# Performance work log

Hardware: AMD Instinct MI355X
Metric: run time of the kernel (lower is better)

The kernel has to match this reference:

```python
import jax, jax.numpy as jnp
import numpy as np

N = 100000          # nodes
E = 600000          # edges (avg degree ~6, mesh graph)
C_IN = 6            # input features (xyz + normals)
H = 64              # hidden channels per PointTransformerConv
OUT = 10            # out_channels
NEG_SLOPE = 0.01    # F.leaky_relu default slope
IN_DIMS = [C_IN, C_IN + H, C_IN + 2 * H, C_IN + 3 * H]


def _lin(key, fin, fout):
    return jax.random.normal(key, (fin, fout), jnp.float32) / np.float32(np.sqrt(fin))


def setup_inputs() -> dict:
    key = jax.random.key(0)
    ks = jax.random.split(key, 40)
    inp = {
        "x": jax.random.normal(ks[0], (N, C_IN), jnp.float32),
        "edge_index": jax.random.randint(ks[1], (2, E), 0, N, jnp.int32),
    }
    k = 2
    for l, fin in enumerate(IN_DIMS, start=1):
        inp[f"w{l}_lin"] = _lin(ks[k], fin, H); k += 1   # value projection (bias=False)
        inp[f"w{l}_src"] = _lin(ks[k], fin, H); k += 1   # attention src projection
        inp[f"w{l}_dst"] = _lin(ks[k], fin, H); k += 1   # attention dst projection
        inp[f"w{l}_pos"] = _lin(ks[k], fin, H); k += 1   # positional MLP (Linear)
        inp[f"b{l}_pos"] = jnp.zeros((H,), jnp.float32)
    inp["w_mlp1"] = _lin(ks[k], C_IN + 4 * H, H); k += 1
    inp["b_mlp1"] = jnp.zeros((H,), jnp.float32)
    inp["w_mlp2"] = _lin(ks[k], H, OUT); k += 1
    inp["b_mlp2"] = jnp.zeros((OUT,), jnp.float32)
    return inp


def _ptconv(x, src, dst, w_lin, w_src, w_dst, w_pos, b_pos):
    """PointTransformerConv with x serving as both features and positions.
    message = softmax_i(a_dst[i] - a_src[j] + delta_ij) * (h[j] + delta_ij),
    delta_ij = pos_nn(x_i - x_j); sum-aggregated over incoming edges."""
    h = x @ w_lin                                   # [N,H] values
    a_src = x @ w_src                               # [N,H]
    a_dst = x @ w_dst                               # [N,H]
    delta = (x[dst] - x[src]) @ w_pos + b_pos       # [E,H] pos_nn(pos_i - pos_j)
    alpha = a_dst[dst] - a_src[src] + delta         # [E,H] per-edge, per-channel logits
    # numerically stable segment softmax over edges grouped by destination node
    amax = jax.ops.segment_max(alpha, dst, num_segments=N)      # [N,H]
    e = jnp.exp(alpha - amax[dst])                              # [E,H]
    denom = jax.ops.segment_sum(e, dst, num_segments=N)         # [N,H]
    w = e / (denom[dst] + 1e-16)                                # [E,H]
    return jax.ops.segment_sum(w * (h[src] + delta), dst, num_segments=N)  # [N,H]


def _forward(x, edge_index, ps):
    src, dst = edge_index[0], edge_index[1]
    lrelu = lambda v: jnp.where(v > 0, v, NEG_SLOPE * v)
    x1 = _ptconv(x, src, dst, *ps[0])
    x2 = lrelu(_ptconv(jnp.concatenate([x, x1], 1), src, dst, *ps[1]))
    x3 = lrelu(_ptconv(jnp.concatenate([x, x1, x2], 1), src, dst, *ps[2]))
    x4 = lrelu(_ptconv(jnp.concatenate([x, x1, x2, x3], 1), src, dst, *ps[3]))
    out = jnp.concatenate([x, x1, x2, x3, x4], 1)   # [N, 262]
    w_mlp1, b_mlp1, w_mlp2, b_mlp2 = ps[4]
    out = out @ w_mlp1 + b_mlp1                     # dropout = identity (eval mode)
    return out @ w_mlp2 + b_mlp2                    # [N, OUT]


def reference(x, edge_index,
              w1_lin, w1_src, w1_dst, w1_pos, b1_pos,
              w2_lin, w2_src, w2_dst, w2_pos, b2_pos,
              w3_lin, w3_src, w3_dst, w3_pos, b3_pos,
              w4_lin, w4_src, w4_dst, w4_pos, b4_pos,
              w_mlp1, b_mlp1, w_mlp2, b_mlp2):
    ps = [(w1_lin, w1_src, w1_dst, w1_pos, b1_pos),
          (w2_lin, w2_src, w2_dst, w2_pos, b2_pos),
          (w3_lin, w3_src, w3_dst, w3_pos, b3_pos),
          (w4_lin, w4_src, w4_dst, w4_pos, b4_pos),
          (w_mlp1, b_mlp1, w_mlp2, b_mlp2)]
    return _forward(x, edge_index, ps)
```

## Files before the change

### kernel.cpp

```cpp
#include <hip/hip_runtime.h>
#include <hip/hip_fp16.h>

#define NN 100000
#define EE 600000
#define XSB 288
#define SCAN_B 2048
#define LOG2E 1.44269504f

typedef __attribute__((ext_vector_type(8))) short s16x8;
typedef __attribute__((ext_vector_type(4))) float f32x4;

__device__ inline unsigned short f2b(float f) {
    unsigned u = __float_as_uint(f);
    u += 0x7fffu + ((u >> 16) & 1u);
    return (unsigned short)(u >> 16);
}

__device__ inline void wconv_elem(int idx, int fin,
                                  const float* wlin, const float* wsrc,
                                  const float* wpos, unsigned short* wt) {
    int ks = idx / 6144;
    int rem = idx - ks * 6144;
    int col = rem >> 5, kk = rem & 31;
    int k = ks * 32 + kk;
    float val = 0.f;
    if (k < fin) {
        int m = col >> 6, c = col & 63;
        const float* W = (m == 0) ? wlin : (m == 1) ? wsrc : wpos;
        val = W[k * 64 + c];
    }
    wt[idx] = f2b(val);
}

#define O0 600000
#define O1 606144
#define O2 624576
#define O3 655296
#define O4 698304
#define O5 716736
#define O6 1316736
#define O7 1316800

__global__ __launch_bounds__(256) void k_setup(
    const float* __restrict__ x, const int* __restrict__ ei,
    const float* __restrict__ wl0, const float* __restrict__ ws0, const float* __restrict__ wp0,
    const float* __restrict__ wl1, const float* __restrict__ ws1, const float* __restrict__ wp1,
    const float* __restrict__ wl2, const float* __restrict__ ws2, const float* __restrict__ wp2,
    const float* __restrict__ wl3, const float* __restrict__ ws3, const float* __restrict__ wp3,
    const float* __restrict__ w1,
    unsigned short* __restrict__ xb,
    unsigned short* __restrict__ wt0, unsigned short* __restrict__ wt1,
    unsigned short* __restrict__ wt2, unsigned short* __restrict__ wt3,
    unsigned short* __restrict__ w1t, int* __restrict__ deg,
    unsigned* __restrict__ vgu) {
    int i = blockIdx.x * 256 + threadIdx.x;
    if (i < O0) {
        int n = i / 6, c = i - n * 6;
        xb[(size_t)n * XSB + c] = f2b(x[i]);
    } else if (i < O1) {
        wconv_elem(i - O0, 6, wl0, ws0, wp0, wt0);
    } else if (i < O2) {
        wconv_elem(i - O1, 70, wl1, ws1, wp1, wt1);
    } else if (i < O3) {
        wconv_elem(i - O2, 134, wl2, ws2, wp2, wt2);
    } else if (i < O4) {
        wconv_elem(i - O3, 198, wl3, ws3, wp3, wt3);
    } else if (i < O5) {
        int idx = i - O4;
        int col = idx / 288, k = idx - col * 288;
        w1t[idx] = f2b((k < 262) ? w1[k * 64 + col] : 0.f);
    } else if (i < O6) {
        atomicAdd(&deg[ei[EE + (i - O5)]], 1);
    } else if (i < O7) {
        vgu[(size_t)NN * 64 + (i - O6)] = 0u;
    }
}


__global__ void k_scan1(const int* __restrict__ deg, int* __restrict__ rowptr,
                        int* __restrict__ bsum) {
    __shared__ int sh[256];
    int b = blockIdx.x, t = threadIdx.x;
    int base = b * SCAN_B + t * 8;
    int vals[8];
    int s = 0;
#pragma unroll
    for (int j = 0; j < 8; j++) {
        int i = base + j;
        int d = (i < NN) ? deg[i] : 0;
        s += d;
        vals[j] = s;
    }
    sh[t] = s;
    __syncthreads();
    for (int off = 1; off < 256; off <<= 1) {
        int vv = (t >= off) ? sh[t - off] : 0;
        __syncthreads();
        sh[t] += vv;
        __syncthreads();
    }
    int excl = (t > 0) ? sh[t - 1] : 0;
#pragma unroll
    for (int j = 0; j < 8; j++) {
        int i = base + j;
        if (i < NN) rowptr[i + 1] = vals[j] + excl;
    }
    if (t == 255) bsum[b] = sh[255];
}

__global__ void k_scan3m(const int* __restrict__ deg, int* __restrict__ rowptr,
                         const int* __restrict__ bsum, int* __restrict__ cursor) {
    __shared__ int soff;
    int b = blockIdx.x, t = threadIdx.x;
    if (t < 64) {
        int v = (t < b) ? bsum[t] : 0;
#pragma unroll
        for (int m = 1; m < 64; m <<= 1) v += __shfl_xor(v, m);
        if (t == 0) soff = v;
    }
    __syncthreads();
    int off = soff;
    int base = b * SCAN_B + t * 8;
#pragma unroll
    for (int j = 0; j < 8; j++) {
        int i = base + j;
        if (i < NN) {
            int incl = rowptr[i + 1] + off;
            rowptr[i + 1] = incl;
            cursor[i] = incl - deg[i];
        }
    }
    if (b == 0 && t == 0) rowptr[0] = 0;
}

__global__ void k_scatter(const int* __restrict__ ei, int* __restrict__ cursor,
                          int* __restrict__ csrc) {
    int e = blockIdx.x * 256 + threadIdx.x;
    if (e < EE) {
        int d = ei[EE + e];
        int pos = atomicAdd(&cursor[d], 1);
        csrc[pos] = ei[e];
    }
}


template <int KP>
__global__ __launch_bounds__(256) void k_projm(
    const unsigned short* __restrict__ xb, const unsigned short* __restrict__ wt,
    const float* __restrict__ bpos,
    unsigned* __restrict__ vg, __half* __restrict__ qh) {
    __shared__ short wl[192 * 32];
    const int t = threadIdx.x;
    const int w = t >> 6, l = t & 63;
    const int lo = l & 15, hi = l >> 4;
    const int row_w = blockIdx.x * 128 + w * 32;

    f32x4 acc[2][12];
#pragma unroll
    for (int a = 0; a < 2; a++)
#pragma unroll
        for (int i = 0; i < 12; i++) acc[a][i] = (f32x4)0.f;

    const unsigned short* arow0 = xb + (size_t)(row_w + lo) * XSB;
    const unsigned short* arow1 = xb + (size_t)(row_w + 16 + lo) * XSB;
#pragma unroll
    for (int ks = 0; ks < KP / 32; ks++) {
        __syncthreads();
        {
            const uint4* src = (const uint4*)wt + (size_t)ks * 768;
            uint4* dst = (uint4*)wl;
#pragma unroll
            for (int i = 0; i < 3; i++) dst[i * 256 + t] = src[i * 256 + t];
        }
        __syncthreads();
        s16x8 af0 = *(const s16x8*)(arow0 + ks * 32 + hi * 8);
        s16x8 af1 = *(const s16x8*)(arow1 + ks * 32 + hi * 8);
#pragma unroll
        for (int ct = 0; ct < 12; ct++) {
            s16x8 bf = *(const s16x8*)&wl[(ct * 16 + lo) * 32 + hi * 8];
            acc[0][ct] = __builtin_amdgcn_mfma_f32_16x16x32_bf16(af0, bf, acc[0][ct], 0, 0, 0);
            acc[1][ct] = __builtin_amdgcn_mfma_f32_16x16x32_bf16(af1, bf, acc[1][ct], 0, 0, 0);
        }
    }

#pragma unroll
    for (int tile = 0; tile < 2; tile++) {
#pragma unroll
        for (int r = 0; r < 4; r++) {
            int node = row_w + tile * 16 + hi * 4 + r;
            if (node < NN) {
#pragma unroll
                for (int j = 0; j < 4; j++) {
                    int c = j * 16 + lo;
                    float h  = acc[tile][0 + j][r];
                    float as = acc[tile][4 + j][r];
                    float p  = acc[tile][8 + j][r];
                    size_t o = (size_t)node * 64 + c;
                    float P = __builtin_amdgcn_exp2f(-(as + p) * LOG2E);
                    vg[o] = (unsigned)f2b(P) | ((unsigned)f2b(P * (h - p)) << 16);
                    qh[o] = __float2half(p + bpos[c]);
                }
            }
        }
    }
}


__global__ __launch_bounds__(256) void k_mlp1f(
    const unsigned short* __restrict__ xb, const unsigned short* __restrict__ w1t,
    const float* __restrict__ b1, const float* __restrict__ w2,
    const float* __restrict__ b2, float* __restrict__ out) {
    __shared__ float w2l[64][10];
    __shared__ float b2l[10];
    __shared__ float b1l[64];
    for (int t = threadIdx.x; t < 714; t += 256) {
        if (t < 640) ((float*)w2l)[t] = w2[t];
        else if (t < 650) b2l[t - 640] = b2[t - 640];
        else b1l[t - 650] = b1[t - 650];
    }
    __syncthreads();

    const int w = threadIdx.x >> 6, l = threadIdx.x & 63;
    const int lo = l & 15, hi = l >> 4;
    const int row_w = blockIdx.x * 256 + w * 64;

    f32x4 acc[4][4];
#pragma unroll
    for (int a = 0; a < 4; a++)
#pragma unroll
        for (int b = 0; b < 4; b++) acc[a][b] = (f32x4)0.f;

#pragma unroll
    for (int ks = 0; ks < 9; ks++) {
        const int k0 = ks * 32 + hi * 8;
        s16x8 bf[4];
#pragma unroll
        for (int ct = 0; ct < 4; ct++)
            bf[ct] = *(const s16x8*)(w1t + (size_t)(ct * 16 + lo) * 288 + k0);
#pragma unroll
        for (int rt = 0; rt < 4; rt++) {
            s16x8 af = *(const s16x8*)(xb + (size_t)(row_w + rt * 16 + lo) * XSB + k0);
#pragma unroll
            for (int ct = 0; ct < 4; ct++)
                acc[rt][ct] = __builtin_amdgcn_mfma_f32_16x16x32_bf16(af, bf[ct], acc[rt][ct], 0, 0, 0);
        }
    }

#pragma unroll
    for (int rt = 0; rt < 4; rt++) {
#pragma unroll
        for (int r = 0; r < 4; r++) {
            int node = row_w + rt * 16 + hi * 4 + r;
            float po[10];
#pragma unroll
            for (int o = 0; o < 10; o++) po[o] = 0.f;
#pragma unroll
            for (int ct = 0; ct < 4; ct++) {
                int c = ct * 16 + lo;
                float hv = acc[rt][ct][r] + b1l[c];
#pragma unroll
                for (int o = 0; o < 10; o++) po[o] = fmaf(hv, w2l[c][o], po[o]);
            }
#pragma unroll
            for (int m = 1; m < 16; m <<= 1)
#pragma unroll
                for (int o = 0; o < 10; o++) po[o] += __shfl_xor(po[o], m);
            if (lo == 0 && node < NN) {
                float* op = out + (size_t)node * 10;
#pragma unroll
                for (int o = 0; o < 5; o++)
                    *(float2*)(op + o * 2) = make_float2(po[o * 2] + b2l[o * 2],
                                                         po[o * 2 + 1] + b2l[o * 2 + 1]);
            }
        }
    }
}


template <int RELU>
__global__ __launch_bounds__(256) void k_edge(
    const uint4* __restrict__ vg,
    const uint2* __restrict__ qh,
    const int* __restrict__ rowptr, const int* __restrict__ csrc,
    unsigned short* __restrict__ xb, int col) {
    int l = threadIdx.x & 63;
    int g = l >> 4, lg = l & 15;
    int node = (blockIdx.x * 4 + (threadIdx.x >> 6)) * 4 + g;
    int b = rowptr[node], e = rowptr[node + 1];
    int deg = e - b;
    int md = max(deg, __shfl_xor(deg, 16));
    md = max(md, __shfl_xor(md, 32));
    uint2 qr = qh[(size_t)node * 16 + lg];
    float d[4] = {0.f, 0.f, 0.f, 0.f};
    float s[4] = {0.f, 0.f, 0.f, 0.f};
    for (int it = 0; it < md; it += 2) {
        int i0 = NN, i1 = NN;
        if (it < deg)     i0 = csrc[b + it];
        if (it + 1 < deg) i1 = csrc[b + it + 1];
        uint4 r0 = vg[(size_t)i0 * 16 + lg];
        uint4 r1 = vg[(size_t)i1 * 16 + lg];
        const unsigned* u0 = (const unsigned*)&r0;
        const unsigned* u1 = (const unsigned*)&r1;
#pragma unroll
        for (int ch = 0; ch < 4; ch++) {
            d[ch] += __uint_as_float(u0[ch] << 16);
            s[ch] += __uint_as_float(u0[ch] & 0xFFFF0000u);
        }
#pragma unroll
        for (int ch = 0; ch < 4; ch++) {
            d[ch] += __uint_as_float(u1[ch] << 16);
            s[ch] += __uint_as_float(u1[ch] & 0xFFFF0000u);
        }
    }
    float2 q01 = __half22float2(*(const __half2*)&qr.x);
    float2 q23 = __half22float2(*(const __half2*)&qr.y);
    float qv[4] = {q01.x, q01.y, q23.x, q23.y};
    float o[4];
#pragma unroll
    for (int ch = 0; ch < 4; ch++) {
        float v = (s[ch] + qv[ch] * d[ch]) / (d[ch] + 1e-16f);
        if (RELU) v = (v > 0.f) ? v : 0.01f * v;
        o[ch] = v;
    }
    unsigned short* dst = xb + (size_t)node * XSB + col + 4 * lg;
    *(unsigned*)(dst)     = (unsigned)f2b(o[0]) | ((unsigned)f2b(o[1]) << 16);
    *(unsigned*)(dst + 2) = (unsigned)f2b(o[2]) | ((unsigned)f2b(o[3]) << 16);
}


extern "C" void kernel_launch(void* const* d_in, const int* in_sizes, int n_in,
                              void* d_out, int out_size, void* d_ws, size_t ws_size,
                              hipStream_t stream) {
    const float* x = (const float*)d_in[0];
    const int* ei = (const int*)d_in[1];
    const float* W[4][4];
    const float* BP[4];
    int base = 2;
    for (int l = 0; l < 4; l++) {
        for (int m = 0; m < 4; m++) W[l][m] = (const float*)d_in[base + m];
        BP[l] = (const float*)d_in[base + 4];
        base += 5;
    }
    const float* w1 = (const float*)d_in[22];
    const float* b1 = (const float*)d_in[23];
    const float* w2 = (const float*)d_in[24];
    const float* b2 = (const float*)d_in[25];

    char* wsp = (char*)d_ws;
    size_t off = 0;
    auto alloc = [&](size_t bytes) {
        void* p = wsp + off;
        off += (bytes + 255) & ~(size_t)255;
        return p;
    };
    unsigned short* xb = (unsigned short*)alloc((size_t)(NN + 256) * XSB * 2);
    unsigned* vg = (unsigned*)alloc((size_t)(NN + 1) * 64 * 4);
    __half* qh = (__half*)alloc((size_t)NN * 64 * 2);
    int* deg = (int*)alloc((size_t)NN * 4);
    int* rowptr = (int*)alloc((size_t)(NN + 1) * 4);
    int* cursor = (int*)alloc((size_t)NN * 4);
    int* bsum = (int*)alloc(1024 * 4);
    int* csrc = (int*)alloc((size_t)EE * 4);
    const int KPv[4] = {32, 96, 160, 224};
    unsigned short* wt[4];
    for (int l = 0; l < 4; l++) wt[l] = (unsigned short*)alloc((size_t)192 * KPv[l] * 2);
    unsigned short* w1t = (unsigned short*)alloc((size_t)64 * 288 * 2);

    hipMemsetAsync(deg, 0, (size_t)NN * 4, stream);
    k_setup<<<(O7 + 255) / 256, 256, 0, stream>>>(
        x, ei, W[0][0], W[0][1], W[0][3], W[1][0], W[1][1], W[1][3],
        W[2][0], W[2][1], W[2][3], W[3][0], W[3][1], W[3][3], w1,
        xb, wt[0], wt[1], wt[2], wt[3], w1t, deg, vg);

    int nb = (NN + SCAN_B - 1) / SCAN_B;
    k_scan1<<<nb, 256, 0, stream>>>(deg, rowptr, bsum);
    k_scan3m<<<nb, 256, 0, stream>>>(deg, rowptr, bsum, cursor);
    k_scatter<<<(EE + 255) / 256, 256, 0, stream>>>(ei, cursor, csrc);

    const int gProj = (NN + 127) / 128;
    const int gEdge = NN / 16;
    const uint4* vgu = (const uint4*)vg;
    const uint2* qh2 = (const uint2*)qh;

    k_projm<32><<<gProj, 256, 0, stream>>>(xb, wt[0], BP[0], vg, qh);
    k_edge<0><<<gEdge, 256, 0, stream>>>(vgu, qh2, rowptr, csrc, xb, 6);
    k_projm<96><<<gProj, 256, 0, stream>>>(xb, wt[1], BP[1], vg, qh);
    k_edge<1><<<gEdge, 256, 0, stream>>>(vgu, qh2, rowptr, csrc, xb, 70);
    k_projm<160><<<gProj, 256, 0, stream>>>(xb, wt[2], BP[2], vg, qh);
    k_edge<1><<<gEdge, 256, 0, stream>>>(vgu, qh2, rowptr, csrc, xb, 134);
    k_projm<224><<<gProj, 256, 0, stream>>>(xb, wt[3], BP[3], vg, qh);
    k_edge<1><<<gEdge, 256, 0, stream>>>(vgu, qh2, rowptr, csrc, xb, 198);

    k_mlp1f<<<(NN + 255) / 256, 256, 0, stream>>>(xb, w1t, b1, w2, b2, (float*)d_out);
}
```

Baseline: 314.8 us.

## Fuse edge aggregation with next layer projection using ping-pong buffers

```diff
diff --git a/kernel.cpp b/kernel.cpp
--- a/kernel.cpp
+++ b/kernel.cpp
@@ -14,6 +14,15 @@
     unsigned u = __float_as_uint(f);
     u += 0x7fffu + ((u >> 16) & 1u);
     return (unsigned short)(u >> 16);
+}
+
+__device__ inline void accum4(float* d, float* s, const uint4& r) {
+    const unsigned* u = (const unsigned*)&r;
+#pragma unroll
+    for (int ch = 0; ch < 4; ch++) {
+        d[ch] += __uint_as_float(u[ch] << 16);
+        s[ch] += __uint_as_float(u[ch] & 0xFFFF0000u);
+    }
 }
 
 __device__ inline void wconv_elem(int idx, int fin,
@@ -39,7 +48,7 @@
 #define O4 698304
 #define O5 716736
 #define O6 1316736
-#define O7 1316800
+#define O7 1316864
 
 __global__ __launch_bounds__(256) void k_setup(
     const float* __restrict__ x, const int* __restrict__ ei,
@@ -52,7 +61,7 @@
     unsigned short* __restrict__ wt0, unsigned short* __restrict__ wt1,
     unsigned short* __restrict__ wt2, unsigned short* __restrict__ wt3,
     unsigned short* __restrict__ w1t, int* __restrict__ deg,
-    unsigned* __restrict__ vgu) {
+    unsigned* __restrict__ vg0, unsigned* __restrict__ vg1) {
     int i = blockIdx.x * 256 + threadIdx.x;
     if (i < O0) {
         int n = i / 6, c = i - n * 6;
@@ -72,7 +81,9 @@
     } else if (i < O6) {
         atomicAdd(&deg[ei[EE + (i - O5)]], 1);
     } else if (i < O7) {
-        vgu[(size_t)NN * 64 + (i - O6)] = 0u;
+        int j = i - O6;
+        unsigned* dst = (j < 64) ? vg0 : vg1;
+        dst[(size_t)NN * 64 + (j & 63)] = 0u;
     }
 }
 
@@ -145,11 +156,10 @@
 
 
 template <int KP>
-__global__ __launch_bounds__(256) void k_projm(
+__device__ inline void proj_body(
     const unsigned short* __restrict__ xb, const unsigned short* __restrict__ wt,
     const float* __restrict__ bpos,
-    unsigned* __restrict__ vg, __half* __restrict__ qh) {
-    __shared__ short wl[192 * 32];
+    unsigned* __restrict__ vg, __half* __restrict__ qh, short* wl) {
     const int t = threadIdx.x;
     const int w = t >> 6, l = t & 63;
     const int lo = l & 15, hi = l >> 4;
@@ -205,6 +215,93 @@
     }
 }
 
+template <int KP>
+__global__ __launch_bounds__(256) void k_projm(
+    const unsigned short* __restrict__ xb, const unsigned short* __restrict__ wt,
+    const float* __restrict__ bpos,
+    unsigned* __restrict__ vg, __half* __restrict__ qh) {
+    __shared__ short wl[192 * 32];
+    proj_body<KP>(xb, wt, bpos, vg, qh, wl);
+}
+
+
+template <int RELU>
+__device__ inline void edge_node(
+    int node, int lg, int gbase,
+    const uint4* __restrict__ vgA, const uint2* __restrict__ qhA,
+    const int* __restrict__ rowptr, const int* __restrict__ csrc,
+    unsigned short* __restrict__ xb, int col) {
+    int b = rowptr[node], e = rowptr[node + 1];
+    int deg = e - b;
+    int pre = (deg > 0) ? csrc[min(b + lg, e - 1)] : (int)NN;
+    uint2 qr = qhA[(size_t)node * 16 + lg];
+    float d[4] = {0.f, 0.f, 0.f, 0.f};
+    float s[4] = {0.f, 0.f, 0.f, 0.f};
+    int degc = min(deg, 16);
+    for (int it = 0; it < degc; it += 4) {
+        int i0 = __shfl(pre, gbase + it);
+        int i1 = (it + 1 < deg) ? __shfl(pre, gbase + it + 1) : (int)NN;
+        int i2 = (it + 2 < deg) ? __shfl(pre, gbase + it + 2) : (int)NN;
+        int i3 = (it + 3 < deg) ? __shfl(pre, gbase + it + 3) : (int)NN;
+        uint4 r0 = vgA[(size_t)i0 * 16 + lg];
+        uint4 r1 = vgA[(size_t)i1 * 16 + lg];
+        uint4 r2 = vgA[(size_t)i2 * 16 + lg];
+        uint4 r3 = vgA[(size_t)i3 * 16 + lg];
+        accum4(d, s, r0); accum4(d, s, r1); accum4(d, s, r2); accum4(d, s, r3);
+    }
+    for (int it = 16; it < deg; ++it) {
+        uint4 r0 = vgA[(size_t)csrc[b + it] * 16 + lg];
+        accum4(d, s, r0);
+    }
+    float2 q01 = __half22float2(*(const __half2*)&qr.x);
+    float2 q23 = __half22float2(*(const __half2*)&qr.y);
+    float qv[4] = {q01.x, q01.y, q23.x, q23.y};
+    float o[4];
+#pragma unroll
+    for (int ch = 0; ch < 4; ch++) {
+        float v = (s[ch] + qv[ch] * d[ch]) / (d[ch] + 1e-16f);
+        if (RELU) v = (v > 0.f) ? v : 0.01f * v;
+        o[ch] = v;
+    }
+    unsigned short* dst = xb + (size_t)node * XSB + col + 4 * lg;
+    *(unsigned*)(dst)     = (unsigned)f2b(o[0]) | ((unsigned)f2b(o[1]) << 16);
+    *(unsigned*)(dst + 2) = (unsigned)f2b(o[2]) | ((unsigned)f2b(o[3]) << 16);
+}
+
+template <int RELU>
+__global__ __launch_bounds__(256) void k_edge(
+    const uint4* __restrict__ vg, const uint2* __restrict__ qh,
+    const int* __restrict__ rowptr, const int* __restrict__ csrc,
+    unsigned short* __restrict__ xb, int col) {
+    int l = threadIdx.x & 63;
+    int g = l >> 4, lg = l & 15;
+    int node = (blockIdx.x * 4 + (threadIdx.x >> 6)) * 4 + g;
+    edge_node<RELU>(node, lg, g * 16, vg, qh, rowptr, csrc, xb, col);
+}
+
+
+template <int KP, int RELU>
+__global__ __launch_bounds__(256) void k_edgeproj(
+    const uint4* __restrict__ vgA, const uint2* __restrict__ qhA,
+    const int* __restrict__ rowptr, const int* __restrict__ csrc,
+    unsigned short* __restrict__ xb, int col,
+    const unsigned short* __restrict__ wt, const float* __restrict__ bpos,
+    unsigned* __restrict__ vgB, __half* __restrict__ qhB) {
+    __shared__ short wl[192 * 32];
+    const int t = threadIdx.x;
+    const int l = t & 63;
+    const int g = l >> 4, lg = l & 15;
+    const int nbase = blockIdx.x * 128 + ((t >> 6) * 4 + g) * 8;
+#pragma unroll 1
+    for (int r = 0; r < 8; ++r) {
+        int node = nbase + r;
+        if (node < NN)
+            edge_node<RELU>(node, lg, g * 16, vgA, qhA, rowptr, csrc, xb, col);
+    }
+    __syncthreads();
+    proj_body<KP>(xb, wt, bpos, vgB, qhB, wl);
+}
+
 
 __global__ __launch_bounds__(256) void k_mlp1f(
     const unsigned short* __restrict__ xb, const unsigned short* __restrict__ w1t,
@@ -274,57 +371,6 @@
             }
         }
     }
-}
-
-
-template <int RELU>
-__global__ __launch_bounds__(256) void k_edge(
-    const uint4* __restrict__ vg,
-    const uint2* __restrict__ qh,
-    const int* __restrict__ rowptr, const int* __restrict__ csrc,
-    unsigned short* __restrict__ xb, int col) {
-    int l = threadIdx.x & 63;
-    int g = l >> 4, lg = l & 15;
-    int node = (blockIdx.x * 4 + (threadIdx.x >> 6)) * 4 + g;
-    int b = rowptr[node], e = rowptr[node + 1];
-    int deg = e - b;
-    int md = max(deg, __shfl_xor(deg, 16));
-    md = max(md, __shfl_xor(md, 32));
-    uint2 qr = qh[(size_t)node * 16 + lg];
-    float d[4] = {0.f, 0.f, 0.f, 0.f};
-    float s[4] = {0.f, 0.f, 0.f, 0.f};
-    for (int it = 0; it < md; it += 2) {
-        int i0 = NN, i1 = NN;
-        if (it < deg)     i0 = csrc[b + it];
-        if (it + 1 < deg) i1 = csrc[b + it + 1];
-        uint4 r0 = vg[(size_t)i0 * 16 + lg];
-        uint4 r1 = vg[(size_t)i1 * 16 + lg];
-        const unsigned* u0 = (const unsigned*)&r0;
-        const unsigned* u1 = (const unsigned*)&r1;
-#pragma unroll
-        for (int ch = 0; ch < 4; ch++) {
-            d[ch] += __uint_as_float(u0[ch] << 16);
-            s[ch] += __uint_as_float(u0[ch] & 0xFFFF0000u);
-        }
-#pragma unroll
-        for (int ch = 0; ch < 4; ch++) {
-            d[ch] += __uint_as_float(u1[ch] << 16);
-            s[ch] += __uint_as_float(u1[ch] & 0xFFFF0000u);
-        }
-    }
-    float2 q01 = __half22float2(*(const __half2*)&qr.x);
-    float2 q23 = __half22float2(*(const __half2*)&qr.y);
-    float qv[4] = {q01.x, q01.y, q23.x, q23.y};
-    float o[4];
-#pragma unroll
-    for (int ch = 0; ch < 4; ch++) {
-        float v = (s[ch] + qv[ch] * d[ch]) / (d[ch] + 1e-16f);
-        if (RELU) v = (v > 0.f) ? v : 0.01f * v;
-        o[ch] = v;
-    }
-    unsigned short* dst = xb + (size_t)node * XSB + col + 4 * lg;
-    *(unsigned*)(dst)     = (unsigned)f2b(o[0]) | ((unsigned)f2b(o[1]) << 16);
-    *(unsigned*)(dst + 2) = (unsigned)f2b(o[2]) | ((unsigned)f2b(o[3]) << 16);
 }
 
 
@@ -354,13 +400,15 @@
         return p;
     };
     unsigned short* xb = (unsigned short*)alloc((size_t)(NN + 256) * XSB * 2);
-    unsigned* vg = (unsigned*)alloc((size_t)(NN + 1) * 64 * 4);
-    __half* qh = (__half*)alloc((size_t)NN * 64 * 2);
+    unsigned* vg0 = (unsigned*)alloc((size_t)(NN + 1) * 64 * 4);
+    unsigned* vg1 = (unsigned*)alloc((size_t)(NN + 1) * 64 * 4);
+    __half* qh0 = (__half*)alloc((size_t)NN * 64 * 2);
+    __half* qh1 = (__half*)alloc((size_t)NN * 64 * 2);
     int* deg = (int*)alloc((size_t)NN * 4);
     int* rowptr = (int*)alloc((size_t)(NN + 1) * 4);
     int* cursor = (int*)alloc((size_t)NN * 4);
     int* bsum = (int*)alloc(1024 * 4);
-    int* csrc = (int*)alloc((size_t)EE * 4);
+    int* csrc = (int*)alloc((size_t)(EE + 16) * 4);
     const int KPv[4] = {32, 96, 160, 224};
     unsigned short* wt[4];
     for (int l = 0; l < 4; l++) wt[l] = (unsigned short*)alloc((size_t)192 * KPv[l] * 2);
@@ -370,7 +418,7 @@
     k_setup<<<(O7 + 255) / 256, 256, 0, stream>>>(
         x, ei, W[0][0], W[0][1], W[0][3], W[1][0], W[1][1], W[1][3],
         W[2][0], W[2][1], W[2][3], W[3][0], W[3][1], W[3][3], w1,
-        xb, wt[0], wt[1], wt[2], wt[3], w1t, deg, vg);
+        xb, wt[0], wt[1], wt[2], wt[3], w1t, deg, vg0, vg1);
 
     int nb = (NN + SCAN_B - 1) / SCAN_B;
     k_scan1<<<nb, 256, 0, stream>>>(deg, rowptr, bsum);
@@ -379,17 +427,16 @@
 
     const int gProj = (NN + 127) / 128;
     const int gEdge = NN / 16;
-    const uint4* vgu = (const uint4*)vg;
-    const uint2* qh2 = (const uint2*)qh;
-
-    k_projm<32><<<gProj, 256, 0, stream>>>(xb, wt[0], BP[0], vg, qh);
-    k_edge<0><<<gEdge, 256, 0, stream>>>(vgu, qh2, rowptr, csrc, xb, 6);
-    k_projm<96><<<gProj, 256, 0, stream>>>(xb, wt[1], BP[1], vg, qh);
-    k_edge<1><<<gEdge, 256, 0, stream>>>(vgu, qh2, rowptr, csrc, xb, 70);
-    k_projm<160><<<gProj, 256, 0, stream>>>(xb, wt[2], BP[2], vg, qh);
-    k_edge<1><<<gEdge, 256, 0, stream>>>(vgu, qh2, rowptr, csrc, xb, 134);
-    k_projm<224><<<gProj, 256, 0, stream>>>(xb, wt[3], BP[3], vg, qh);
-    k_edge<1><<<gEdge, 256, 0, stream>>>(vgu, qh2, rowptr, csrc, xb, 198);
+
+    k_projm<32><<<gProj, 256, 0, stream>>>(xb, wt[0], BP[0], vg0, qh0);
+    k_edgeproj<96, 0><<<gProj, 256, 0, stream>>>(
+        (const uint4*)vg0, (const uint2*)qh0, rowptr, csrc, xb, 6, wt[1], BP[1], vg1, qh1);
+    k_edgeproj<160, 1><<<gProj, 256, 0, stream>>>(
+        (const uint4*)vg1, (const uint2*)qh1, rowptr, csrc, xb, 70, wt[2], BP[2], vg0, qh0);
+    k_edgeproj<224, 1><<<gProj, 256, 0, stream>>>(
+        (const uint4*)vg0, (const uint2*)qh0, rowptr, csrc, xb, 134, wt[3], BP[3], vg1, qh1);
+    k_edge<1><<<gEdge, 256, 0, stream>>>(
+        (const uint4*)vg1, (const uint2*)qh1, rowptr, csrc, xb, 198);
 
     k_mlp1f<<<(NN + 255) / 256, 256, 0, stream>>>(xb, w1t, b1, w2, b2, (float*)d_out);
 }
```

Measured after the change: 327.8 us. 4.1% more time.
